# Kernel tuning notes

Hardware: AMD Instinct MI355X
Metric: run time of the kernel (lower is better)

The kernel has to match this reference:

```python
import math
import jax, jax.numpy as jnp
import numpy as np


def setup_inputs() -> dict:
    key = jax.random.key(0)
    k1, k2, k3, k4 = jax.random.split(key, 4)
    B, C, H, W = 8, 256, 128, 128
    norm_dim, K = 64, 3
    return {
        "fea": jax.random.normal(k1, (B, C, H, W), dtype=jnp.float32),
        "norm_feat": jax.random.normal(k2, (B, norm_dim, 1, 1), dtype=jnp.float32),
        "mod_w": jax.random.normal(k3, (C, norm_dim, 1, 1), dtype=jnp.float32),
        "mod_b": jnp.zeros((C,), dtype=jnp.float32),
        "weight": jax.random.normal(k4, (1, C, C, K, K), dtype=jnp.float32),
    }


def reference(fea, norm_feat, mod_w, mod_b, weight):
    B, C, H, W = fea.shape
    K = weight.shape[-1]
    scale = 1.0 / math.sqrt(C * K * K)
    # 1x1 modulation conv on (B, norm_dim, 1, 1) -> style (B, C)
    style = jnp.einsum('bdhw,cd->bc', norm_feat, mod_w[:, :, 0, 0]) + mod_b  # (B, C)
    # modulate: (1, C_out, C_in, K, K) * (B, 1, C_in, 1, 1)
    w = scale * weight * style[:, None, :, None, None]  # (B, C, C, K, K)
    demod = jax.lax.rsqrt(jnp.sum(w * w, axis=(2, 3, 4)) + 1e-8)  # (B, C)
    w = w * demod[:, :, None, None, None]
    # grouped-conv trick: groups=B, input (1, B*C, H, W), weight (B*C, C, K, K)
    w = w.reshape(B * C, C, K, K)
    x = fea.reshape(1, B * C, H, W)
    out = jax.lax.conv_general_dilated(
        x, w,
        window_strides=(1, 1),
        padding=[(K // 2, K // 2), (K // 2, K // 2)],
        dimension_numbers=('NCHW', 'OIHW', 'NCHW'),
        feature_group_count=B,
    )
    return out.reshape(B, C, H, W)
```

## Files before the change

### kernel.cpp

```cpp
#include <hip/hip_runtime.h>

typedef unsigned short u16;
typedef unsigned int u32;
typedef short s8v __attribute__((ext_vector_type(8)));
typedef float f16v __attribute__((ext_vector_type(16)));
typedef u32 u32x4 __attribute__((ext_vector_type(4)));

__device__ __forceinline__ u16 f2bf(float f) {
    u32 u = __float_as_uint(f);
    u += 0x7FFFu + ((u >> 16) & 1u);
    return (u16)(u >> 16);
}

__device__ __forceinline__ void async_load16(const u16* g, u16* l) {
    __builtin_amdgcn_global_load_lds(
        (const __attribute__((address_space(1))) u32*)g,
        (__attribute__((address_space(3))) u32*)l,
        16, 0, 0);
}

__global__ void style_kernel(const float* __restrict__ norm_feat,
                             const float* __restrict__ mod_w,
                             const float* __restrict__ mod_b,
                             float* __restrict__ style) {
    __shared__ float nf[64];
    __shared__ float mw[256][65];
    const int b = blockIdx.x;
    const int tid = threadIdx.x;

    if (tid < 64) nf[tid] = norm_feat[b * 64 + tid];
    #pragma unroll
    for (int i = 0; i < 64; ++i) {
        int idx = i * 256 + tid;
        mw[idx >> 6][idx & 63] = mod_w[idx];
    }
    __syncthreads();

    float s = mod_b[tid];
    #pragma unroll 8
    for (int d = 0; d < 64; ++d) s += nf[d] * mw[tid][d];
    style[b * 256 + tid] = s;
}

__global__ void modulate_kernel(const float* __restrict__ style,
                                const float* __restrict__ weight,
                                u16* __restrict__ Wmod) {
    const int co = blockIdx.x;
    const int b  = blockIdx.y;
    const int ci = threadIdx.x;

    __shared__ float red[256];

    const float s = style[b * 256 + ci];

    float w9[9];
    const float* wp = weight + ((size_t)co * 256 + ci) * 9;
    float sq = 0.f;
    #pragma unroll
    for (int t = 0; t < 9; ++t) { w9[t] = wp[t]; sq += w9[t] * w9[t]; }

    red[ci] = sq * s * s;
    __syncthreads();
    for (int off = 128; off > 0; off >>= 1) {
        if (ci < off) red[ci] += red[ci + off];
        __syncthreads();
    }
    const float scale = 1.0f / 48.0f;
    const float demod = rsqrtf(scale * scale * red[0] + 1e-8f);
    const float coef  = scale * s * demod;

    const size_t tile = (((size_t)b * 9 * 8 + (co >> 5)) * 16 + (ci >> 4)) * 512
                      + (size_t)((co & 31) + 32 * ((ci >> 3) & 1)) * 8 + (ci & 7);
    #pragma unroll
    for (int t = 0; t < 9; ++t) {
        Wmod[tile + (size_t)t * 65536] = f2bf(w9[t] * coef);
    }
}

__global__ __launch_bounds__(256) void transpose_kernel(const float* __restrict__ fea,
                                                        u16* __restrict__ feaT) {
    __shared__ float lds_t[64][132];
    const int y = blockIdx.x;
    const int b = blockIdx.y;
    const int tid = threadIdx.x;

    for (int c0 = 0; c0 < 256; c0 += 64) {
        #pragma unroll
        for (int r = 0; r < 8; ++r) {
            int i  = r * 256 + tid;
            int c  = i >> 5;
            int x4 = i & 31;
            float4 v = *(const float4*)&fea[(((size_t)(b * 256 + c0 + c)) * 128 + y) * 128 + x4 * 4];
            *(float4*)&lds_t[c][x4 * 4] = v;
        }
        __syncthreads();
        #pragma unroll
        for (int jj = 0; jj < 4; ++jj) {
            int p   = jj * 256 + tid;
            int x   = p & 127;
            int g   = p >> 7;
            int cb8 = g * 8;
            u32x4 wv;
            #pragma unroll
            for (int k = 0; k < 4; ++k) {
                float f0 = lds_t[cb8 + 2 * k][x];
                float f1 = lds_t[cb8 + 2 * k + 1][x];
                wv[k] = (u32)f2bf(f0) | ((u32)f2bf(f1) << 16);
            }
            int c  = c0 + cb8;
            int ch = c >> 4;
            int cg = (c >> 3) & 1;
            size_t off = (((((size_t)b * 128 + y) * 16 + ch) * 2 + cg) * 128 + x) * 8;
            *(u32x4*)&feaT[off] = wv;
        }
        __syncthreads();
    }
}

__global__ __launch_bounds__(256) void conv_mfma(
        const u16* __restrict__ Wmod,
        const u16* __restrict__ feaT,
        float* __restrict__ out) {
    __shared__ u16 lds[2][3][2][128][8];
    __shared__ u16 zpad[8];

    const int lin = blockIdx.x + 128 * (blockIdx.y + 2 * blockIdx.z);
    const int nid = (lin & 7) * 256 + (lin >> 3);
    const int y   = nid & 127;
    const int cbk = (nid >> 7) & 1;
    const int b   = nid >> 8;

    const int tid  = threadIdx.x;
    const int lane = tid & 63;
    const int wave = tid >> 6;
    const int mw  = wave & 1;
    const int nw  = wave >> 1;
    const int l31 = lane & 31;
    const int l5  = lane >> 5;

    if (tid < 8) zpad[tid] = 0;

    const bool rok0 = (y > 0);
    const bool rok2 = (y < 127);

    const u16* Abase = Wmod + (size_t)b * 9 * 65536
                            + (size_t)(cbk * 4 + mw * 2) * 8192 + (size_t)lane * 8;

    auto loadA = [&](int t, int i, int ch) -> s8v {
        return *(const s8v*)(Abase + (size_t)t * 65536 + (size_t)i * 8192 + (size_t)ch * 512);
    };

    auto stage = [&](int buf, int ch) {
        u16* ldsb = &lds[buf][0][0][0][0];
        #pragma unroll
        for (int i = 0; i < 3; ++i) {
            int u  = wave + 4 * i;
            int r  = u >> 2;
            int cg = (u >> 1) & 1;
            int xq = u & 1;
            int gy = y - 1 + r;
            if ((unsigned)gy < 128u) {
                const u16* g = feaT +
                    (((((size_t)b * 128 + gy) * 16 + ch) * 2 + cg) * 128 + xq * 64) * 8
                    + (size_t)lane * 8;
                async_load16(g, ldsb + ((r * 2 + cg) * 128 + xq * 64) * 8);
            }
        }
    };

    f16v acc[2][2];
    #pragma unroll
    for (int i = 0; i < 2; ++i)
        #pragma unroll
        for (int j = 0; j < 2; ++j) acc[i][j] = (f16v)0.0f;

    s8v afrA[2], afrB[2];

    stage(0, 0);
    #pragma unroll
    for (int i = 0; i < 2; ++i) afrA[i] = loadA(0, i, 0);
    __syncthreads();

    const int xb0 = nw * 64 + l31 - 1;

    auto chunk_body = [&](int ch, s8v (&cur)[2], s8v (&alt)[2]) {
        const u16* bufp = &lds[ch & 1][0][0][0][0];
        #pragma unroll
        for (int t = 0; t < 9; ++t) {
            if (t < 8) {
                if (t & 1) {
                    #pragma unroll
                    for (int i = 0; i < 2; ++i) cur[i] = loadA(t + 1, i, ch);
                } else {
                    #pragma unroll
                    for (int i = 0; i < 2; ++i) alt[i] = loadA(t + 1, i, ch);
                }
            } else if (ch < 15) {
                #pragma unroll
                for (int i = 0; i < 2; ++i) alt[i] = loadA(0, i, ch + 1);
            }

            const int kh = t / 3, kw = t % 3;
            const bool rok = (kh == 0) ? rok0 : (kh == 2 ? rok2 : true);

            s8v bfr[2];
            #pragma unroll
            for (int j = 0; j < 2; ++j) {
                int x_in = xb0 + j * 32 + kw;
                bool v = rok && ((unsigned)x_in < 128u);
                const u16* bp = v ? (bufp + (((kh * 2 + l5) * 128 + x_in) * 8)) : zpad;
                bfr[j] = *(const s8v*)bp;
            }

            if ((t & 1) == 0) {
                #pragma unroll
                for (int i = 0; i < 2; ++i)
                    #pragma unroll
                    for (int j = 0; j < 2; ++j)
                        acc[i][j] = __builtin_amdgcn_mfma_f32_32x32x16_bf16(
                            cur[i], bfr[j], acc[i][j], 0, 0, 0);
            } else {
                #pragma unroll
                for (int i = 0; i < 2; ++i)
                    #pragma unroll
                    for (int j = 0; j < 2; ++j)
                        acc[i][j] = __builtin_amdgcn_mfma_f32_32x32x16_bf16(
                            alt[i], bfr[j], acc[i][j], 0, 0, 0);
            }

            if (t == 4 && ch < 15) stage((ch + 1) & 1, ch + 1);
        }
    };

    #pragma unroll 1
    for (int m = 0; m < 8; ++m) {
        chunk_body(2 * m, afrA, afrB);
        __syncthreads();
        chunk_body(2 * m + 1, afrB, afrA);
        __syncthreads();
    }

    const int x_base = nw * 64 + l31;
    #pragma unroll
    for (int i = 0; i < 2; ++i) {
        #pragma unroll
        for (int j = 0; j < 2; ++j) {
            #pragma unroll
            for (int reg = 0; reg < 16; ++reg) {
                int co = cbk * 128 + mw * 64 + i * 32 + (reg & 3) + 8 * (reg >> 2) + 4 * l5;
                out[(((size_t)(b * 256 + co) * 128 + y) * 128) + x_base + j * 32] = acc[i][j][reg];
            }
        }
    }
}

extern "C" void kernel_launch(void* const* d_in, const int* in_sizes, int n_in,
                              void* d_out, int out_size, void* d_ws, size_t ws_size,
                              hipStream_t stream) {
    const float* fea       = (const float*)d_in[0];
    const float* norm_feat = (const float*)d_in[1];
    const float* mod_w     = (const float*)d_in[2];
    const float* mod_b     = (const float*)d_in[3];
    const float* weight    = (const float*)d_in[4];
    float* out = (float*)d_out;

    u16* Wmod = (u16*)d_ws;
    u16* feaT = (u16*)((char*)d_ws + 9u * 1024u * 1024u);
    float* style = (float*)feaT;

    style_kernel<<<dim3(8), 256, 0, stream>>>(norm_feat, mod_w, mod_b, style);
    modulate_kernel<<<dim3(256, 8), 256, 0, stream>>>(style, weight, Wmod);
    transpose_kernel<<<dim3(128, 8), 256, 0, stream>>>(fea, feaT);
    conv_mfma<<<dim3(128, 2, 8), 256, 0, stream>>>(Wmod, feaT, out);
}
```

Baseline: 391.2 us.

## Compute two output rows per block sharing staged input rows across waves

Each conv block now covers two output rows with 8 waves instead of one row with 4 waves, staging 4 input rows per channel chunk instead of 3, so input halo rows are reused across both output rows. The A-fragment prefetch changes from a two-buffer alternation to a three-deep rotating register ring that runs further ahead. This cuts LDS staging traffic per output row and halves the grid, but raises threads per block. Weight fragments are still loaded per wave, so weight traffic is unchanged.

```diff
diff --git a/kernel.cpp b/kernel.cpp
--- a/kernel.cpp
+++ b/kernel.cpp
@@ -117,31 +117,32 @@
     }
 }
 
-__global__ __launch_bounds__(256) void conv_mfma(
+__global__ __launch_bounds__(512, 4) void conv_mfma(
         const u16* __restrict__ Wmod,
         const u16* __restrict__ feaT,
         float* __restrict__ out) {
-    __shared__ u16 lds[2][3][2][128][8];
+    __shared__ u16 lds[2][4][2][128][8];
     __shared__ u16 zpad[8];
 
-    const int lin = blockIdx.x + 128 * (blockIdx.y + 2 * blockIdx.z);
-    const int nid = (lin & 7) * 256 + (lin >> 3);
-    const int y   = nid & 127;
-    const int cbk = (nid >> 7) & 1;
-    const int b   = nid >> 8;
+    const int lin = blockIdx.x + 64 * (blockIdx.y + 2 * blockIdx.z);
+    const int nid = (lin & 7) * 128 + (lin >> 3);
+    const int yp  = nid & 63;
+    const int cbk = (nid >> 6) & 1;
+    const int b   = nid >> 7;
 
     const int tid  = threadIdx.x;
     const int lane = tid & 63;
     const int wave = tid >> 6;
     const int mw  = wave & 1;
-    const int nw  = wave >> 1;
+    const int nw  = (wave >> 1) & 1;
+    const int yw  = wave >> 2;
     const int l31 = lane & 31;
     const int l5  = lane >> 5;
 
     if (tid < 8) zpad[tid] = 0;
 
-    const bool rok0 = (y > 0);
-    const bool rok2 = (y < 127);
+    const int y_out = 2 * yp + yw;
+    const bool rokv[3] = { (y_out > 0), true, (y_out < 127) };
 
     const u16* Abase = Wmod + (size_t)b * 9 * 65536
                             + (size_t)(cbk * 4 + mw * 2) * 8192 + (size_t)lane * 8;
@@ -153,12 +154,12 @@
     auto stage = [&](int buf, int ch) {
         u16* ldsb = &lds[buf][0][0][0][0];
         #pragma unroll
-        for (int i = 0; i < 3; ++i) {
-            int u  = wave + 4 * i;
+        for (int i = 0; i < 2; ++i) {
+            int u  = wave + 8 * i;
             int r  = u >> 2;
             int cg = (u >> 1) & 1;
             int xq = u & 1;
-            int gy = y - 1 + r;
+            int gy = 2 * yp - 1 + r;
             if ((unsigned)gy < 128u) {
                 const u16* g = feaT +
                     (((((size_t)b * 128 + gy) * 16 + ch) * 2 + cg) * 128 + xq * 64) * 8
@@ -174,69 +175,53 @@
         #pragma unroll
         for (int j = 0; j < 2; ++j) acc[i][j] = (f16v)0.0f;
 
-    s8v afrA[2], afrB[2];
+    s8v fr[3][2];
 
     stage(0, 0);
     #pragma unroll
-    for (int i = 0; i < 2; ++i) afrA[i] = loadA(0, i, 0);
+    for (int g = 0; g < 3; ++g) {
+        fr[g][0] = loadA(g, 0, 0);
+        fr[g][1] = loadA(g, 1, 0);
+    }
     __syncthreads();
 
     const int xb0 = nw * 64 + l31 - 1;
 
-    auto chunk_body = [&](int ch, s8v (&cur)[2], s8v (&alt)[2]) {
+    #pragma unroll 1
+    for (int ch = 0; ch < 16; ++ch) {
         const u16* bufp = &lds[ch & 1][0][0][0][0];
         #pragma unroll
         for (int t = 0; t < 9; ++t) {
-            if (t < 8) {
-                if (t & 1) {
-                    #pragma unroll
-                    for (int i = 0; i < 2; ++i) cur[i] = loadA(t + 1, i, ch);
-                } else {
-                    #pragma unroll
-                    for (int i = 0; i < 2; ++i) alt[i] = loadA(t + 1, i, ch);
-                }
-            } else if (ch < 15) {
-                #pragma unroll
-                for (int i = 0; i < 2; ++i) alt[i] = loadA(0, i, ch + 1);
-            }
-
             const int kh = t / 3, kw = t % 3;
-            const bool rok = (kh == 0) ? rok0 : (kh == 2 ? rok2 : true);
+            const int rr = kh + yw;
+            const bool rok = rokv[kh];
 
             s8v bfr[2];
             #pragma unroll
             for (int j = 0; j < 2; ++j) {
                 int x_in = xb0 + j * 32 + kw;
                 bool v = rok && ((unsigned)x_in < 128u);
-                const u16* bp = v ? (bufp + (((kh * 2 + l5) * 128 + x_in) * 8)) : zpad;
+                const u16* bp = v ? (bufp + (((rr * 2 + l5) * 128 + x_in) * 8)) : zpad;
                 bfr[j] = *(const s8v*)bp;
             }
 
-            if ((t & 1) == 0) {
+            #pragma unroll
+            for (int i = 0; i < 2; ++i)
                 #pragma unroll
-                for (int i = 0; i < 2; ++i)
-                    #pragma unroll
-                    for (int j = 0; j < 2; ++j)
-                        acc[i][j] = __builtin_amdgcn_mfma_f32_32x32x16_bf16(
-                            cur[i], bfr[j], acc[i][j], 0, 0, 0);
-            } else {
-                #pragma unroll
-                for (int i = 0; i < 2; ++i)
-                    #pragma unroll
-                    for (int j = 0; j < 2; ++j)
-                        acc[i][j] = __builtin_amdgcn_mfma_f32_32x32x16_bf16(
-                            alt[i], bfr[j], acc[i][j], 0, 0, 0);
-            }
-
-            if (t == 4 && ch < 15) stage((ch + 1) & 1, ch + 1);
-        }
-    };
-
-    #pragma unroll 1
-    for (int m = 0; m < 8; ++m) {
-        chunk_body(2 * m, afrA, afrB);
-        __syncthreads();
-        chunk_body(2 * m + 1, afrB, afrA);
+                for (int j = 0; j < 2; ++j)
+                    acc[i][j] = __builtin_amdgcn_mfma_f32_32x32x16_bf16(
+                        fr[t % 3][i], bfr[j], acc[i][j], 0, 0, 0);
+
+            if (t < 6) {
+                fr[t % 3][0] = loadA(t + 3, 0, ch);
+                fr[t % 3][1] = loadA(t + 3, 1, ch);
+            } else if (ch < 15) {
+                fr[t % 3][0] = loadA(t - 6, 0, ch + 1);
+                fr[t % 3][1] = loadA(t - 6, 1, ch + 1);
+            }
+
+            if (t == 3 && ch < 15) stage((ch + 1) & 1, ch + 1);
+        }
         __syncthreads();
     }
 
@@ -248,7 +233,7 @@
             #pragma unroll
             for (int reg = 0; reg < 16; ++reg) {
                 int co = cbk * 128 + mw * 64 + i * 32 + (reg & 3) + 8 * (reg >> 2) + 4 * l5;
-                out[(((size_t)(b * 256 + co) * 128 + y) * 128) + x_base + j * 32] = acc[i][j][reg];
+                out[(((size_t)(b * 256 + co) * 128 + y_out) * 128) + x_base + j * 32] = acc[i][j][reg];
             }
         }
     }
@@ -271,5 +256,5 @@
     style_kernel<<<dim3(8), 256, 0, stream>>>(norm_feat, mod_w, mod_b, style);
     modulate_kernel<<<dim3(256, 8), 256, 0, stream>>>(style, weight, Wmod);
     transpose_kernel<<<dim3(128, 8), 256, 0, stream>>>(fea, feaT);
-    conv_mfma<<<dim3(128, 2, 8), 256, 0, stream>>>(Wmod, feaT, out);
-}
+    conv_mfma<<<dim3(64, 2, 8), 512, 0, stream>>>(Wmod, feaT, out);
+}
```

New measurement: 386.2 us. No clear change (-1.3%).
